# Kernel optimization log

Hardware: AMD Instinct MI355X
Metric: run time of the kernel (lower is better)

## Reference

```python
import jax, jax.numpy as jnp
import numpy as np

B, N, T, F_IN, F_OUT = 4, 2048, 12, 32, 32
ALPHA = 0.2  # leaky relu negative slope
NEG_INF = -9e15


def setup_inputs() -> dict:
    key = jax.random.key(0)
    k = jax.random.split(key, 6)
    x = jax.random.normal(k[0], (B, N, T, F_IN), dtype=jnp.float32)
    adj = jax.random.randint(k[1], (N, N), 0, 2, dtype=jnp.int32)
    W = jax.random.normal(k[2], (T * F_IN, T * F_OUT), dtype=jnp.float32) * 0.05
    a = jax.random.normal(k[3], (2 * T * F_OUT, 1), dtype=jnp.float32) * 0.05
    conv_w = jax.random.normal(k[4], (T, T, 3), dtype=jnp.float32) * 0.1  # (out_ch, in_ch, k)
    conv_b = jnp.zeros((T,), dtype=jnp.float32)
    return {"x": x, "adj": adj, "W": W, "a": a, "conv_w": conv_w, "conv_b": conv_b}


def reference(x, adj, W, a, conv_w, conv_b):
    Bz, Nn, Tt, Fi = x.shape
    Fo = W.shape[1] // Tt
    # temporal conv: channels = timesteps, length = nodes*features
    xt = x.transpose(0, 2, 1, 3).reshape(Bz, Tt, Nn * Fi)  # (B,T,L)
    xt = jax.lax.conv_general_dilated(
        xt, conv_w, window_strides=(1,), padding=[(1, 1)],
        dimension_numbers=("NCH", "OIH", "NCH")) + conv_b[None, :, None]
    xt = xt.reshape(Bz, Tt, Nn, Fi).transpose(0, 2, 1, 3).reshape(Bz, Nn, Tt * Fi)
    Wh = xt @ W  # (B, N, T*Fo)
    # e[b,i,j] = leakyrelu(Wh[b,i].a1 + Wh[b,j].a2)  -- avoids O(N^2 * 2F) concat
    a1 = a[: Tt * Fo, 0]
    a2 = a[Tt * Fo:, 0]
    f1 = Wh @ a1  # (B, N)
    f2 = Wh @ a2  # (B, N)
    e = jax.nn.leaky_relu(f1[:, :, None] + f2[:, None, :], negative_slope=ALPHA)
    e = jnp.where(adj[None, :, :] > 0, e, NEG_INF)
    attn = jax.nn.softmax(e, axis=-1)  # (B, N, N); dropout omitted (eval mode)
    h_prime = attn @ Wh  # (B, N, T*Fo)
    return jax.nn.elu(h_prime).reshape(Bz, Nn, Tt, Fo)
```

## Files before the change

kernel.cpp:

```cpp
#include <hip/hip_runtime.h>

using short8 = __attribute__((ext_vector_type(8))) short;
using f32x4  = __attribute__((ext_vector_type(4))) float;
using f32x16 = __attribute__((ext_vector_type(16))) float;

__device__ __forceinline__ unsigned short f2bf(float f) {
  unsigned u = __float_as_uint(f);
  u += 0x7fffu + ((u >> 16) & 1u);
  return (unsigned short)(u >> 16);
}

__global__ __launch_bounds__(256) void conv_kernel(const float* __restrict__ x,
                                                   const float* __restrict__ cw,
                                                   const float* __restrict__ cb,
                                                   unsigned short* __restrict__ xt) {
  __shared__ float tile[12][264];
  __shared__ float cws[432];
  __shared__ float cbs[12];
  const int b  = blockIdx.y;
  const int p0 = blockIdx.x << 8;
  const int tid = threadIdx.x;
  for (int i = tid; i < 432; i += 256) cws[i] = cw[i];
  if (tid < 12) cbs[tid] = cb[tid];
  for (int t = 0; t < 12; ++t) {
    for (int i = tid; i < 258; i += 256) {
      int gp = p0 + i - 1;
      float v = 0.f;
      if (gp >= 0 && gp < 2048 * 32) {
        int n = gp >> 5, f = gp & 31;
        v = x[(((size_t)b * 2048 + n) * 12 + t) * 32 + f];
      }
      tile[t][i] = v;
    }
  }
  __syncthreads();
  float acc[12];
#pragma unroll
  for (int to = 0; to < 12; ++to) acc[to] = cbs[to];
#pragma unroll
  for (int ti = 0; ti < 12; ++ti) {
    float x0 = tile[ti][tid], x1 = tile[ti][tid + 1], x2 = tile[ti][tid + 2];
#pragma unroll
    for (int to = 0; to < 12; ++to) {
      const float* wp = &cws[(to * 12 + ti) * 3];
      acc[to] += x0 * wp[0] + x1 * wp[1] + x2 * wp[2];
    }
  }
  const int p = p0 + tid, n = p >> 5, f = p & 31;
  unsigned short* op = xt + ((size_t)b * 2048 + n) * 384 + f;
#pragma unroll
  for (int to = 0; to < 12; ++to) op[to * 32] = f2bf(acc[to]);
}

__global__ __launch_bounds__(256) void transpose_f2b_kernel(const float* __restrict__ in,
                                                            unsigned short* __restrict__ out,
                                                            int rows, int cols) {
  __shared__ float tile[32][33];
  const int r0 = blockIdx.x * 32, c0 = blockIdx.y * 32;
  const int li = threadIdx.x >> 5, ci = threadIdx.x & 31;
#pragma unroll
  for (int p = 0; p < 4; ++p) {
    int r = li + p * 8;
    tile[r][ci] = in[(size_t)(r0 + r) * cols + c0 + ci];
  }
  __syncthreads();
#pragma unroll
  for (int p = 0; p < 4; ++p) {
    int c = li + p * 8;
    out[(size_t)(c0 + c) * rows + r0 + ci] = f2bf(tile[ci][c]);
  }
}

__global__ __launch_bounds__(256) void adjmask_kernel(const int* __restrict__ adj,
                                                      unsigned* __restrict__ adjm) {
  const int wv = (blockIdx.x << 2) + (threadIdx.x >> 6);
  const int lane = threadIdx.x & 63;
  const int row = wv >> 5, j0 = (wv & 31) << 6;
  unsigned long long mask = __ballot(adj[(size_t)row * 2048 + j0 + lane] > 0);
  if (lane == 0) {
    adjm[row * 64 + (j0 >> 5)]     = (unsigned)mask;
    adjm[row * 64 + (j0 >> 5) + 1] = (unsigned)(mask >> 32);
  }
}

__global__ __launch_bounds__(384) void gemm_wh_kernel(const unsigned short* __restrict__ xt,
                                                      const unsigned short* __restrict__ Wt,
                                                      const float* __restrict__ a,
                                                      unsigned short* __restrict__ whb,
                                                      float* __restrict__ f1,
                                                      float* __restrict__ f2) {
  __shared__ float s1s[16], s2s[16];
  const int tid = threadIdx.x;
  const int r0 = blockIdx.x << 4;
  const int w = tid >> 6;
  const int lane = tid & 63;
  const int il = lane & 15, kg = lane >> 4;
  if (tid < 16) { s1s[tid] = 0.f; s2s[tid] = 0.f; }
  __syncthreads();
  f32x4 acc[4];
#pragma unroll
  for (int t = 0; t < 4; ++t) acc[t] = (f32x4){0.f, 0.f, 0.f, 0.f};
  const unsigned short* ap = xt + (size_t)(r0 + il) * 384 + kg * 8;
#pragma unroll
  for (int kk = 0; kk < 12; ++kk) {
    short8 af = *reinterpret_cast<const short8*>(ap + kk * 32);
#pragma unroll
    for (int t = 0; t < 4; ++t) {
      int c = (w << 6) + (t << 4) + il;
      short8 bf = *reinterpret_cast<const short8*>(Wt + (size_t)c * 384 + kk * 32 + kg * 8);
      acc[t] = __builtin_amdgcn_mfma_f32_16x16x32_bf16(af, bf, acc[t], 0, 0, 0);
    }
  }
  float p1[4] = {0.f, 0.f, 0.f, 0.f}, p2[4] = {0.f, 0.f, 0.f, 0.f};
#pragma unroll
  for (int t = 0; t < 4; ++t) {
    const int c = (w << 6) + (t << 4) + il;
    const float a1v = a[c], a2v = a[384 + c];
#pragma unroll
    for (int r = 0; r < 4; ++r) { p1[r] += acc[t][r] * a1v; p2[r] += acc[t][r] * a2v; }
  }
#pragma unroll
  for (int off = 1; off < 16; off <<= 1) {
#pragma unroll
    for (int r = 0; r < 4; ++r) { p1[r] += __shfl_xor(p1[r], off); p2[r] += __shfl_xor(p2[r], off); }
  }
  if (il == 0) {
#pragma unroll
    for (int r = 0; r < 4; ++r) {
      atomicAdd(&s1s[kg * 4 + r], p1[r]);
      atomicAdd(&s2s[kg * 4 + r], p2[r]);
    }
  }
#pragma unroll
  for (int t = 0; t < 4; ++t)
#pragma unroll
    for (int r = 0; r < 4; ++r)
      whb[(size_t)(r0 + kg * 4 + r) * 384 + (w << 6) + (t << 4) + il] = f2bf(acc[t][r]);
  __syncthreads();
  if (tid < 16) { f1[r0 + tid] = s1s[tid]; f2[r0 + tid] = s2s[tid]; }
}

__global__ __launch_bounds__(256) void f2max_kernel(const float* __restrict__ f2,
                                                    float* __restrict__ gmax) {
  __shared__ float wm[4];
  const int b = blockIdx.x;
  const int tid = threadIdx.x;
  float m = -3.0e38f;
  for (int i = tid; i < 2048; i += 256) m = fmaxf(m, f2[b * 2048 + i]);
#pragma unroll
  for (int off = 32; off; off >>= 1) m = fmaxf(m, __shfl_xor(m, off));
  if ((tid & 63) == 0) wm[tid >> 6] = m;
  __syncthreads();
  if (tid == 0) gmax[b] = fmaxf(fmaxf(wm[0], wm[1]), fmaxf(wm[2], wm[3]));
}

__global__ __launch_bounds__(256) void pack_kernel(const unsigned short* __restrict__ whb,
                                                   unsigned short* __restrict__ whp) {
  __shared__ unsigned short ptile[32][392];
  const int b = blockIdx.y;
  const int jg = blockIdx.x;
  const int tid = threadIdx.x;
#pragma unroll
  for (int rep = 0; rep < 6; ++rep) {
    const int flat = rep * 256 + tid;
    const int row = flat / 48, seg = flat - row * 48;
    *reinterpret_cast<short8*>(&ptile[row][seg * 8]) =
        *reinterpret_cast<const short8*>(whb + ((size_t)(b * 2048 + jg * 32 + row)) * 384 + seg * 8);
  }
  __syncthreads();
#pragma unroll
  for (int rep = 0; rep < 6; ++rep) {
    const int flat = rep * 256 + tid;
    const int tile = flat >> 6, l = flat & 63;
    const int ct = tile >> 1, jh = tile & 1;
    const int l5 = l & 31, hw2 = l >> 5;
    short8 v;
#pragma unroll
    for (int e = 0; e < 8; ++e)
      v[e] = (short)ptile[jh * 16 + hw2 * 8 + e][ct * 32 + l5];
    *reinterpret_cast<short8*>((char*)whp +
        ((((size_t)b * 12 + ct) * 128 + jg * 2 + jh) << 10) + l * 16) = v;
  }
}

__global__ __launch_bounds__(256, 2) void attn5_kernel(const float* __restrict__ f1,
                                                       const float* __restrict__ f2,
                                                       const unsigned* __restrict__ adjm,
                                                       const unsigned short* __restrict__ whp,
                                                       const float* __restrict__ gmax,
                                                       float* __restrict__ out) {
  __shared__ float red[4][32][96];
  __shared__ float dred[128];
  const int bi = blockIdx.x;
  const int ch = bi & 1;
  const int b  = (bi & 7) >> 1;
  const int i0 = (bi >> 3) << 5;
  const int tid = threadIdx.x;
  const int ks = tid >> 6;
  const int lane = tid & 63;
  const int l5 = lane & 31, hw = lane >> 5;
  const int ig = i0 + l5;

  const float* f2b = f2 + b * 2048;
  const unsigned* adjr = adjm + (size_t)ig * 64 + ks * 16;
  const float f1v = f1[b * 2048 + ig];
  const float gm = gmax[b];
  const float mz = f1v + gm;
  const float m  = fmaxf(mz, 0.2f * mz);
  const float Az = f1v - m;
  const float Bz = 0.2f * f1v - m;

  const char* wbase = (const char*)whp +
      ((((size_t)b * 12 + ch * 6) * 128 + ks * 32) << 10) + lane * 16;

  const f32x16 zero16 = {0.f,0.f,0.f,0.f,0.f,0.f,0.f,0.f,0.f,0.f,0.f,0.f,0.f,0.f,0.f,0.f};
  f32x16 acc[6];
#pragma unroll
  for (int t = 0; t < 6; ++t) acc[t] = zero16;
  float denom = 0.f;

  short8 bA[6], bB[6];
  float4 fA0, fA1, fB0, fB1;

#define LOADB(DST, KK)                                                                  \
  { _Pragma("unroll")                                                                   \
    for (int tt = 0; tt < 6; ++tt)                                                      \
      DST[tt] = *reinterpret_cast<const short8*>(wbase + (((size_t)tt * 128 + (KK)) << 10)); }
#define LOADF(D0, D1, KK)                                                               \
  { const float* fp_ = f2b + ks * 512 + (KK) * 16 + hw * 8;                             \
    D0 = *(const float4*)fp_; D1 = *(const float4*)(fp_ + 4); }

#define PGEMM(BSET, F0, F1, P01)                                                        \
  { const unsigned bits_ = (awC >> ((P01) * 16 + hw * 8)) & 0xffu;                      \
    const float gv[8] = {F0.x, F0.y, F0.z, F0.w, F1.x, F1.y, F1.z, F1.w};               \
    union { unsigned u[4]; short8 s8; } cc;                                             \
    _Pragma("unroll")                                                                   \
    for (int pr = 0; pr < 4; ++pr) {                                                    \
      const int e = pr * 2;                                                             \
      float plo = ((bits_ >> e) & 1u)                                                   \
          ? __expf(fmaxf(Az + gv[e], fmaf(gv[e], 0.2f, Bz))) : 0.f;                     \
      float phi = ((bits_ >> (e + 1)) & 1u)                                             \
          ? __expf(fmaxf(Az + gv[e + 1], fmaf(gv[e + 1], 0.2f, Bz))) : 0.f;             \
      const unsigned ulo = __float_as_uint(plo) & 0xffff0000u;                          \
      const unsigned uhi = __float_as_uint(phi) & 0xffff0000u;                          \
      denom += __uint_as_float(ulo) + __uint_as_float(uhi);                             \
      cc.u[pr] = uhi | (ulo >> 16);                                                     \
    }                                                                                   \
    _Pragma("unroll")                                                                   \
    for (int qq = 0; qq < 6; ++qq)                                                      \
      acc[qq] = __builtin_amdgcn_mfma_f32_32x32x16_bf16(cc.s8, BSET[qq], acc[qq], 0, 0, 0); }

  LOADB(bA, 0); LOADF(fA0, fA1, 0);
  unsigned awC = adjr[0];

  for (int t = 0; t < 16; ++t) {
    const int k0 = 2 * t;
    const unsigned awN = adjr[t < 15 ? t + 1 : 15];
    LOADB(bB, k0 + 1); LOADF(fB0, fB1, k0 + 1);
    PGEMM(bA, fA0, fA1, 0);
    const int kn = (k0 + 2 < 32) ? k0 + 2 : 31;
    LOADB(bA, kn); LOADF(fA0, fA1, kn);
    PGEMM(bB, fB0, fB1, 1);
    awC = awN;
  }
#undef LOADB
#undef LOADF
#undef PGEMM

  float dn = denom + __shfl_xor(denom, 32);
  if (hw == 0) dred[ks * 32 + l5] = dn;

#pragma unroll
  for (int r = 0; r < 2; ++r) {
#pragma unroll
    for (int t3 = 0; t3 < 3; ++t3) {
      const int t = r * 3 + t3;
#pragma unroll
      for (int q = 0; q < 16; ++q) {
        const int row = (q & 3) + 8 * (q >> 2) + 4 * hw;
        red[ks][row][t3 * 32 + l5] = acc[t][q];
      }
    }
    __syncthreads();
    const size_t ob = ((size_t)b * 2048 + i0) * 384 + ch * 192 + r * 96;
#pragma unroll
    for (int p = 0; p < 12; ++p) {
      const int idx = p * 256 + tid;
      const int row = idx / 96;
      const int c = idx - row * 96;
      float v = red[0][row][c] + red[1][row][c] + red[2][row][c] + red[3][row][c];
      const float d = dred[row] + dred[32 + row] + dred[64 + row] + dred[96 + row];
      v /= d;
      v = v > 0.f ? v : expm1f(v);
      out[ob + (size_t)row * 384 + c] = v;
    }
    __syncthreads();
  }
}

extern "C" void kernel_launch(void* const* d_in, const int* in_sizes, int n_in,
                              void* d_out, int out_size, void* d_ws, size_t ws_size,
                              hipStream_t stream) {
  const float* x  = (const float*)d_in[0];
  const int* adj  = (const int*)d_in[1];
  const float* W  = (const float*)d_in[2];
  const float* a  = (const float*)d_in[3];
  const float* cw = (const float*)d_in[4];
  const float* cb = (const float*)d_in[5];
  float* out = (float*)d_out;

  char* ws = (char*)d_ws;
  unsigned short* xt  = (unsigned short*)ws; ws += (size_t)3145728 * 2;
  unsigned short* Wt  = (unsigned short*)ws; ws += (size_t)147456 * 2;
  unsigned short* Whb = (unsigned short*)ws; ws += (size_t)3145728 * 2;
  unsigned short* whp = (unsigned short*)ws; ws += (size_t)3145728 * 2;
  float* f1           = (float*)ws;          ws += (size_t)8192 * 4;
  float* f2           = (float*)ws;          ws += (size_t)8192 * 4;
  unsigned* adjm      = (unsigned*)ws;       ws += (size_t)2048 * 64 * 4;
  float* gmax         = (float*)ws;          ws += 64;

  conv_kernel<<<dim3(256, 4), 256, 0, stream>>>(x, cw, cb, xt);
  transpose_f2b_kernel<<<dim3(12, 12), 256, 0, stream>>>(W, Wt, 384, 384);
  adjmask_kernel<<<dim3(16384), 256, 0, stream>>>(adj, adjm);
  gemm_wh_kernel<<<dim3(512), 384, 0, stream>>>(xt, Wt, a, Whb, f1, f2);
  f2max_kernel<<<dim3(4), 256, 0, stream>>>(f2, gmax);
  pack_kernel<<<dim3(64, 4), 256, 0, stream>>>(Whb, whp);
  attn5_kernel<<<dim3(512), 256, 0, stream>>>(f1, f2, adjm, whp, gmax, out);
}
```

Baseline: 90.18 us.

## Fuse Wh packing into GEMM epilogue and split attention over more column chunks

```diff
diff --git a/kernel.cpp b/kernel.cpp
--- a/kernel.cpp
+++ b/kernel.cpp
@@ -83,38 +83,42 @@
   }
 }
 
-__global__ __launch_bounds__(384) void gemm_wh_kernel(const unsigned short* __restrict__ xt,
-                                                      const unsigned short* __restrict__ Wt,
-                                                      const float* __restrict__ a,
-                                                      unsigned short* __restrict__ whb,
-                                                      float* __restrict__ f1,
-                                                      float* __restrict__ f2) {
-  __shared__ float s1s[16], s2s[16];
+__global__ __launch_bounds__(512) void gemm_wh2_kernel(const unsigned short* __restrict__ xt,
+                                                       const unsigned short* __restrict__ Wt,
+                                                       const float* __restrict__ a,
+                                                       unsigned short* __restrict__ whp,
+                                                       float* __restrict__ f1,
+                                                       float* __restrict__ f2) {
+  __shared__ unsigned short wtile[32][392];
+  __shared__ float s1s[32], s2s[32];
   const int tid = threadIdx.x;
-  const int r0 = blockIdx.x << 4;
-  const int w = tid >> 6;
-  const int lane = tid & 63;
+  const int rb = blockIdx.x;
+  const int b = rb >> 6, jg = rb & 63;
+  const int r0 = rb << 5;
+  const int w = tid >> 6, lane = tid & 63;
+  const int rg = w >> 2, cg = w & 3;
   const int il = lane & 15, kg = lane >> 4;
-  if (tid < 16) { s1s[tid] = 0.f; s2s[tid] = 0.f; }
-  __syncthreads();
-  f32x4 acc[4];
-#pragma unroll
-  for (int t = 0; t < 4; ++t) acc[t] = (f32x4){0.f, 0.f, 0.f, 0.f};
-  const unsigned short* ap = xt + (size_t)(r0 + il) * 384 + kg * 8;
+  if (tid < 32) { s1s[tid] = 0.f; s2s[tid] = 0.f; }
+  __syncthreads();
+
+  f32x4 acc[6];
+#pragma unroll
+  for (int t = 0; t < 6; ++t) acc[t] = (f32x4){0.f, 0.f, 0.f, 0.f};
+  const unsigned short* ap = xt + (size_t)(r0 + rg * 16 + il) * 384 + kg * 8;
 #pragma unroll
   for (int kk = 0; kk < 12; ++kk) {
     short8 af = *reinterpret_cast<const short8*>(ap + kk * 32);
 #pragma unroll
-    for (int t = 0; t < 4; ++t) {
-      int c = (w << 6) + (t << 4) + il;
+    for (int t = 0; t < 6; ++t) {
+      const int c = cg * 96 + t * 16 + il;
       short8 bf = *reinterpret_cast<const short8*>(Wt + (size_t)c * 384 + kk * 32 + kg * 8);
       acc[t] = __builtin_amdgcn_mfma_f32_16x16x32_bf16(af, bf, acc[t], 0, 0, 0);
     }
   }
   float p1[4] = {0.f, 0.f, 0.f, 0.f}, p2[4] = {0.f, 0.f, 0.f, 0.f};
 #pragma unroll
-  for (int t = 0; t < 4; ++t) {
-    const int c = (w << 6) + (t << 4) + il;
+  for (int t = 0; t < 6; ++t) {
+    const int c = cg * 96 + t * 16 + il;
     const float a1v = a[c], a2v = a[384 + c];
 #pragma unroll
     for (int r = 0; r < 4; ++r) { p1[r] += acc[t][r] * a1v; p2[r] += acc[t][r] * a2v; }
@@ -127,17 +131,31 @@
   if (il == 0) {
 #pragma unroll
     for (int r = 0; r < 4; ++r) {
-      atomicAdd(&s1s[kg * 4 + r], p1[r]);
-      atomicAdd(&s2s[kg * 4 + r], p2[r]);
-    }
-  }
-#pragma unroll
-  for (int t = 0; t < 4; ++t)
+      atomicAdd(&s1s[rg * 16 + kg * 4 + r], p1[r]);
+      atomicAdd(&s2s[rg * 16 + kg * 4 + r], p2[r]);
+    }
+  }
+#pragma unroll
+  for (int t = 0; t < 6; ++t)
 #pragma unroll
     for (int r = 0; r < 4; ++r)
-      whb[(size_t)(r0 + kg * 4 + r) * 384 + (w << 6) + (t << 4) + il] = f2bf(acc[t][r]);
-  __syncthreads();
-  if (tid < 16) { f1[r0 + tid] = s1s[tid]; f2[r0 + tid] = s2s[tid]; }
+      wtile[rg * 16 + kg * 4 + r][cg * 96 + t * 16 + il] = f2bf(acc[t][r]);
+  __syncthreads();
+
+#pragma unroll
+  for (int rep = 0; rep < 3; ++rep) {
+    const int flat = rep * 512 + tid;
+    const int tile = flat >> 6, l = flat & 63;
+    const int ct = tile >> 1, jh = tile & 1;
+    const int l5 = l & 31, hw2 = l >> 5;
+    short8 v;
+#pragma unroll
+    for (int e = 0; e < 8; ++e)
+      v[e] = (short)wtile[jh * 16 + hw2 * 8 + e][ct * 32 + l5];
+    *reinterpret_cast<short8*>((char*)whp +
+        ((((size_t)b * 12 + ct) * 128 + jg * 2 + jh) << 10) + l * 16) = v;
+  }
+  if (tid < 32) { f1[r0 + tid] = s1s[tid]; f2[r0 + tid] = s2s[tid]; }
 }
 
 __global__ __launch_bounds__(256) void f2max_kernel(const float* __restrict__ f2,
@@ -154,36 +172,7 @@
   if (tid == 0) gmax[b] = fmaxf(fmaxf(wm[0], wm[1]), fmaxf(wm[2], wm[3]));
 }
 
-__global__ __launch_bounds__(256) void pack_kernel(const unsigned short* __restrict__ whb,
-                                                   unsigned short* __restrict__ whp) {
-  __shared__ unsigned short ptile[32][392];
-  const int b = blockIdx.y;
-  const int jg = blockIdx.x;
-  const int tid = threadIdx.x;
-#pragma unroll
-  for (int rep = 0; rep < 6; ++rep) {
-    const int flat = rep * 256 + tid;
-    const int row = flat / 48, seg = flat - row * 48;
-    *reinterpret_cast<short8*>(&ptile[row][seg * 8]) =
-        *reinterpret_cast<const short8*>(whb + ((size_t)(b * 2048 + jg * 32 + row)) * 384 + seg * 8);
-  }
-  __syncthreads();
-#pragma unroll
-  for (int rep = 0; rep < 6; ++rep) {
-    const int flat = rep * 256 + tid;
-    const int tile = flat >> 6, l = flat & 63;
-    const int ct = tile >> 1, jh = tile & 1;
-    const int l5 = l & 31, hw2 = l >> 5;
-    short8 v;
-#pragma unroll
-    for (int e = 0; e < 8; ++e)
-      v[e] = (short)ptile[jh * 16 + hw2 * 8 + e][ct * 32 + l5];
-    *reinterpret_cast<short8*>((char*)whp +
-        ((((size_t)b * 12 + ct) * 128 + jg * 2 + jh) << 10) + l * 16) = v;
-  }
-}
-
-__global__ __launch_bounds__(256, 2) void attn5_kernel(const float* __restrict__ f1,
+__global__ __launch_bounds__(256, 3) void attn6_kernel(const float* __restrict__ f1,
                                                        const float* __restrict__ f2,
                                                        const unsigned* __restrict__ adjm,
                                                        const unsigned short* __restrict__ whp,
@@ -192,17 +181,18 @@
   __shared__ float red[4][32][96];
   __shared__ float dred[128];
   const int bi = blockIdx.x;
-  const int ch = bi & 1;
-  const int b  = (bi & 7) >> 1;
-  const int i0 = (bi >> 3) << 5;
+  const int c16 = bi & 15;
+  const int b  = c16 >> 2;
+  const int ch = c16 & 3;
+  const int i0 = (bi >> 4) << 5;
   const int tid = threadIdx.x;
   const int ks = tid >> 6;
   const int lane = tid & 63;
   const int l5 = lane & 31, hw = lane >> 5;
+  const int hw8 = hw * 8;
   const int ig = i0 + l5;
 
   const float* f2b = f2 + b * 2048;
-  const unsigned* adjr = adjm + (size_t)ig * 64 + ks * 16;
   const float f1v = f1[b * 2048 + ig];
   const float gm = gmax[b];
   const float mz = f1v + gm;
@@ -210,29 +200,40 @@
   const float Az = f1v - m;
   const float Bz = 0.2f * f1v - m;
 
+  unsigned awf[16];
+  {
+    const uint4* ap = reinterpret_cast<const uint4*>(adjm + (size_t)ig * 64 + ks * 16);
+#pragma unroll
+    for (int q = 0; q < 4; ++q) {
+      uint4 v = ap[q];
+      awf[4 * q] = v.x; awf[4 * q + 1] = v.y; awf[4 * q + 2] = v.z; awf[4 * q + 3] = v.w;
+    }
+  }
+
   const char* wbase = (const char*)whp +
-      ((((size_t)b * 12 + ch * 6) * 128 + ks * 32) << 10) + lane * 16;
+      ((((size_t)b * 12 + ch * 3) * 128 + ks * 32) << 10) + lane * 16;
 
   const f32x16 zero16 = {0.f,0.f,0.f,0.f,0.f,0.f,0.f,0.f,0.f,0.f,0.f,0.f,0.f,0.f,0.f,0.f};
-  f32x16 acc[6];
-#pragma unroll
-  for (int t = 0; t < 6; ++t) acc[t] = zero16;
+  f32x16 acc[3];
+#pragma unroll
+  for (int t = 0; t < 3; ++t) acc[t] = zero16;
   float denom = 0.f;
 
-  short8 bA[6], bB[6];
-  float4 fA0, fA1, fB0, fB1;
-
-#define LOADB(DST, KK)                                                                  \
+  short8 bfr[3][3];
+  float4 ff[3][2];
+
+#define LOADB(S, KK)                                                                    \
   { _Pragma("unroll")                                                                   \
-    for (int tt = 0; tt < 6; ++tt)                                                      \
-      DST[tt] = *reinterpret_cast<const short8*>(wbase + (((size_t)tt * 128 + (KK)) << 10)); }
-#define LOADF(D0, D1, KK)                                                               \
-  { const float* fp_ = f2b + ks * 512 + (KK) * 16 + hw * 8;                             \
-    D0 = *(const float4*)fp_; D1 = *(const float4*)(fp_ + 4); }
-
-#define PGEMM(BSET, F0, F1, P01)                                                        \
-  { const unsigned bits_ = (awC >> ((P01) * 16 + hw * 8)) & 0xffu;                      \
-    const float gv[8] = {F0.x, F0.y, F0.z, F0.w, F1.x, F1.y, F1.z, F1.w};               \
+    for (int tt = 0; tt < 3; ++tt)                                                      \
+      bfr[S][tt] = *reinterpret_cast<const short8*>(wbase + (((size_t)tt * 128 + (KK)) << 10)); }
+#define LOADF(S, KK)                                                                    \
+  { const float* fp_ = f2b + ks * 512 + (KK) * 16 + hw8;                                \
+    ff[S][0] = *(const float4*)fp_; ff[S][1] = *(const float4*)(fp_ + 4); }
+
+#define PGEMM(S, KK)                                                                    \
+  { const unsigned bits_ = (awf[(KK) >> 1] >> ((((KK) & 1) << 4) + hw8)) & 0xffu;       \
+    const float gv[8] = {ff[S][0].x, ff[S][0].y, ff[S][0].z, ff[S][0].w,                \
+                         ff[S][1].x, ff[S][1].y, ff[S][1].z, ff[S][1].w};               \
     union { unsigned u[4]; short8 s8; } cc;                                             \
     _Pragma("unroll")                                                                   \
     for (int pr = 0; pr < 4; ++pr) {                                                    \
@@ -247,21 +248,19 @@
       cc.u[pr] = uhi | (ulo >> 16);                                                     \
     }                                                                                   \
     _Pragma("unroll")                                                                   \
-    for (int qq = 0; qq < 6; ++qq)                                                      \
-      acc[qq] = __builtin_amdgcn_mfma_f32_32x32x16_bf16(cc.s8, BSET[qq], acc[qq], 0, 0, 0); }
-
-  LOADB(bA, 0); LOADF(fA0, fA1, 0);
-  unsigned awC = adjr[0];
-
-  for (int t = 0; t < 16; ++t) {
-    const int k0 = 2 * t;
-    const unsigned awN = adjr[t < 15 ? t + 1 : 15];
-    LOADB(bB, k0 + 1); LOADF(fB0, fB1, k0 + 1);
-    PGEMM(bA, fA0, fA1, 0);
-    const int kn = (k0 + 2 < 32) ? k0 + 2 : 31;
-    LOADB(bA, kn); LOADF(fA0, fA1, kn);
-    PGEMM(bB, fB0, fB1, 1);
-    awC = awN;
+    for (int qq = 0; qq < 3; ++qq)                                                      \
+      acc[qq] = __builtin_amdgcn_mfma_f32_32x32x16_bf16(cc.s8, bfr[S][qq], acc[qq], 0, 0, 0); }
+
+  LOADB(0, 0); LOADF(0, 0);
+  LOADB(1, 1); LOADF(1, 1);
+#pragma unroll
+  for (int k = 0; k < 32; ++k) {
+    const int s = k % 3;
+    if (k < 30) {
+      const int sn = (k + 2) % 3;
+      LOADB(sn, k + 2); LOADF(sn, k + 2);
+    }
+    PGEMM(s, k);
   }
 #undef LOADB
 #undef LOADF
@@ -269,32 +268,26 @@
 
   float dn = denom + __shfl_xor(denom, 32);
   if (hw == 0) dred[ks * 32 + l5] = dn;
-
-#pragma unroll
-  for (int r = 0; r < 2; ++r) {
-#pragma unroll
-    for (int t3 = 0; t3 < 3; ++t3) {
-      const int t = r * 3 + t3;
-#pragma unroll
-      for (int q = 0; q < 16; ++q) {
-        const int row = (q & 3) + 8 * (q >> 2) + 4 * hw;
-        red[ks][row][t3 * 32 + l5] = acc[t][q];
-      }
-    }
-    __syncthreads();
-    const size_t ob = ((size_t)b * 2048 + i0) * 384 + ch * 192 + r * 96;
-#pragma unroll
-    for (int p = 0; p < 12; ++p) {
-      const int idx = p * 256 + tid;
-      const int row = idx / 96;
-      const int c = idx - row * 96;
-      float v = red[0][row][c] + red[1][row][c] + red[2][row][c] + red[3][row][c];
-      const float d = dred[row] + dred[32 + row] + dred[64 + row] + dred[96 + row];
-      v /= d;
-      v = v > 0.f ? v : expm1f(v);
-      out[ob + (size_t)row * 384 + c] = v;
-    }
-    __syncthreads();
+#pragma unroll
+  for (int t = 0; t < 3; ++t) {
+#pragma unroll
+    for (int q = 0; q < 16; ++q) {
+      const int row = (q & 3) + 8 * (q >> 2) + 4 * hw;
+      red[ks][row][t * 32 + l5] = acc[t][q];
+    }
+  }
+  __syncthreads();
+  const size_t ob = ((size_t)b * 2048 + i0) * 384 + ch * 96;
+#pragma unroll
+  for (int p = 0; p < 12; ++p) {
+    const int idx = p * 256 + tid;
+    const int row = idx / 96;
+    const int c = idx - row * 96;
+    float v = red[0][row][c] + red[1][row][c] + red[2][row][c] + red[3][row][c];
+    const float d = dred[row] + dred[32 + row] + dred[64 + row] + dred[96 + row];
+    v /= d;
+    v = v > 0.f ? v : expm1f(v);
+    out[ob + (size_t)row * 384 + c] = v;
   }
 }
 
@@ -312,7 +305,6 @@
   char* ws = (char*)d_ws;
   unsigned short* xt  = (unsigned short*)ws; ws += (size_t)3145728 * 2;
   unsigned short* Wt  = (unsigned short*)ws; ws += (size_t)147456 * 2;
-  unsigned short* Whb = (unsigned short*)ws; ws += (size_t)3145728 * 2;
   unsigned short* whp = (unsigned short*)ws; ws += (size_t)3145728 * 2;
   float* f1           = (float*)ws;          ws += (size_t)8192 * 4;
   float* f2           = (float*)ws;          ws += (size_t)8192 * 4;
@@ -322,8 +314,7 @@
   conv_kernel<<<dim3(256, 4), 256, 0, stream>>>(x, cw, cb, xt);
   transpose_f2b_kernel<<<dim3(12, 12), 256, 0, stream>>>(W, Wt, 384, 384);
   adjmask_kernel<<<dim3(16384), 256, 0, stream>>>(adj, adjm);
-  gemm_wh_kernel<<<dim3(512), 384, 0, stream>>>(xt, Wt, a, Whb, f1, f2);
+  gemm_wh2_kernel<<<dim3(256), 512, 0, stream>>>(xt, Wt, a, whp, f1, f2);
   f2max_kernel<<<dim3(4), 256, 0, stream>>>(f2, gmax);
-  pack_kernel<<<dim3(64, 4), 256, 0, stream>>>(Whb, whp);
-  attn5_kernel<<<dim3(512), 256, 0, stream>>>(f1, f2, adjm, whp, gmax, out);
-}
+  attn6_kernel<<<dim3(1024), 256, 0, stream>>>(f1, f2, adjm, whp, gmax, out);
+}
```

After: 159.9 us. 77.3% more time.
